# Kernel optimization log

Hardware: AMD Instinct MI355X
Metric: run time of the kernel (lower is better)

Reference implementation:

```python
import jax, jax.numpy as jnp
import numpy as np

B, N, I = 8, 1024, 64
E, H, D = 2, 2, 128   # edge types, heads per layer, hidden dim
O = 64                # num_outputs
IN1 = E * H * D       # layer-1 filter input dim (concat of layer-0 heads)


def setup_inputs() -> dict:
    key = jax.random.key(0)
    ks = jax.random.split(key, 20)
    s = lambda f: 1.0 / np.sqrt(f)
    inp = {
        "nodes": jax.random.normal(ks[0], (B, N, I), jnp.float32),
        "edges": jax.random.normal(ks[1], (B, N, N, E), jnp.float32) * 0.1,
        "Wemb": jax.random.normal(ks[2], (I, D), jnp.float32) * s(I),
        "bemb": jnp.zeros((D,), jnp.float32),
        # layer 0 params: filter W, att nets a1/a2 (weight + bias), state bias
        "W0":   jax.random.normal(ks[3], (E, H, D, D), jnp.float32) * s(D),
        "A1w0": jax.random.normal(ks[4], (E, H, D), jnp.float32) * s(D),
        "A1b0": jnp.zeros((E, H), jnp.float32),
        "A2w0": jax.random.normal(ks[5], (E, H, D), jnp.float32) * s(D),
        "A2b0": jnp.zeros((E, H), jnp.float32),
        "SB0":  jnp.zeros((E, H, D), jnp.float32),
        # layer 1 params (input dim = E*H*D from concat)
        "W1":   jax.random.normal(ks[6], (E, H, IN1, D), jnp.float32) * s(IN1),
        "A1w1": jax.random.normal(ks[7], (E, H, D), jnp.float32) * s(D),
        "A1b1": jnp.zeros((E, H), jnp.float32),
        "A2w1": jax.random.normal(ks[8], (E, H, D), jnp.float32) * s(D),
        "A2b1": jnp.zeros((E, H), jnp.float32),
        "SB1":  jnp.zeros((E, H, D), jnp.float32),
        "Wout": jax.random.normal(ks[9], (D, O), jnp.float32) * s(D),
        "bout": jnp.zeros((O,), jnp.float32),
    }
    return inp


def _gat_layer(state, edges_ebnn, W, a1w, a1b, a2w, a2b, sb):
    # state: (B,N,Fin); W: (E,H,Fin,D); edges_ebnn: (E,1,B,N,N)
    Wh = jnp.einsum('bni,ehid->ehbnd', state, W)                    # (E,H,B,N,D)
    s1 = jnp.einsum('ehbnd,ehd->ehbn', Wh, a1w) + a1b[:, :, None, None]
    s2 = jnp.einsum('ehbnd,ehd->ehbn', Wh, a2w) + a2b[:, :, None, None]
    att = s1[..., :, None] + s2[..., None, :]                       # a1_i + a2_j
    att = jax.nn.leaky_relu(att, 0.2) + edges_ebnn                  # edge-type bias
    att = jax.nn.softmax(att, axis=-2)                              # torch dim=1 (over i)
    msg = jnp.einsum('ehbij,ehbjd->ehbid', att, Wh)                 # bmm aggregation
    return msg + sb[:, :, None, None, :]                            # (E,H,B,N,D)


def reference(nodes, edges, Wemb, bemb,
              W0, A1w0, A1b0, A2w0, A2b0, SB0,
              W1, A1w1, A1b1, A2w1, A2b1, SB1,
              Wout, bout):
    edges_e = jnp.transpose(edges, (3, 0, 1, 2))[:, None]           # (E,1,B,N,N)
    state = jax.nn.relu(nodes @ Wemb + bemb)                        # SlimFC embedding
    # layer 0: concat heads/edgetypes along feature dim (torch order jj outer, ii inner)
    m0 = _gat_layer(state, edges_e, W0, A1w0, A1b0, A2w0, A2b0, SB0)
    state = jnp.transpose(m0, (2, 3, 0, 1, 4)).reshape(B, N, E * H * D)
    # layer 1 (last): elu then mean over all heads/edgetypes
    m1 = jax.nn.elu(_gat_layer(state, edges_e, W1, A1w1, A1b1, A2w1, A2b1, SB1))
    state = jnp.mean(m1, axis=(0, 1))                               # (B,N,D)
    return state @ Wout + bout                                      # (B,N,O)
```

## Files before the change

### kernel.cpp

```cpp
#include <hip/hip_runtime.h>
#include <math.h>

#define NB 8
#define NN 1024
#define NI 64
#define EHC 4
#define ND 128
#define NO 64
#define FIN1 512
#define BN 8192
#define LOG2E 1.4426950408889634f

typedef __attribute__((ext_vector_type(8))) short short8;
typedef __attribute__((ext_vector_type(4))) float f32x4;
typedef __attribute__((ext_vector_type(2))) unsigned uint32x2;

__device__ __forceinline__ unsigned short f2bf(float f) {
    union { float f; unsigned u; } v; v.f = f;
    unsigned r = v.u + 0x7FFF + ((v.u >> 16) & 1);
    return (unsigned short)(r >> 16);
}
__device__ __forceinline__ unsigned short f2h(float f) {
    union { _Float16 h; unsigned short u; } v;
    v.h = (_Float16)f;
    return v.u;
}
__device__ __forceinline__ float h2f(unsigned short u) {
    union { unsigned short u; _Float16 h; } v;
    v.u = u;
    return (float)v.h;
}

__global__ void prepTk(const float* __restrict__ W0, const float* __restrict__ W1,
                       const float* __restrict__ Wemb, const float* __restrict__ Wout,
                       unsigned short* __restrict__ W0T, unsigned short* __restrict__ W1T,
                       unsigned short* __restrict__ WembT, unsigned short* __restrict__ WoutT) {
    int idx = blockIdx.x * 256 + threadIdx.x;
    if (idx < EHC * ND * ND) {
        int eh = idx >> 14, d = (idx >> 7) & 127, k = idx & 127;
        W0T[idx] = f2bf(W0[((size_t)(eh * ND + k)) * ND + d]);
    }
    int idx1 = idx - EHC * ND * ND;
    if (idx1 >= 0 && idx1 < EHC * ND * FIN1) {
        int eh = idx1 >> 16;
        int r = idx1 & 65535;
        int d = r >> 9, k = r & 511;
        W1T[idx1] = f2bf(W1[((size_t)(eh * FIN1 + k)) * ND + d]);
    }
    int idx2 = idx - (EHC * ND * ND + EHC * ND * FIN1);
    if (idx2 >= 0 && idx2 < ND * NI) {
        int d = idx2 >> 6, k = idx2 & 63;
        WembT[idx2] = f2bf(Wemb[k * ND + d]);
    }
    int idx3 = idx - (EHC * ND * ND + EHC * ND * FIN1 + ND * NI);
    if (idx3 >= 0 && idx3 < ND * NO) {
        int o = idx3 >> 7, d = idx3 & 127;
        WoutT[idx3] = f2bf(Wout[d * NO + o]);
    }
}

__global__ __launch_bounds__(256, 4) void embwh0k(
    const float* __restrict__ nodes, const unsigned short* __restrict__ WembT,
    const float* __restrict__ bemb, const unsigned short* __restrict__ W0T,
    unsigned short* __restrict__ WhT, const float* __restrict__ a1w,
    const float* __restrict__ a1b, const float* __restrict__ a2w,
    const float* __restrict__ a2b, float* __restrict__ s1, float* __restrict__ s2) {
    int id = blockIdx.x;
    int g = id & 7, s_ = id >> 3;
    int eh = s_ & 3;
    int row0 = ((s_ >> 2) * 8 + g) * 32;
    int t = threadIdx.x;
    int w = t >> 6, lane = t & 63;
    int m = lane & 15, quad = lane >> 4;

    __shared__ unsigned short stateL[32 * 136];

    f32x4 accE[2][2];
#pragma unroll
    for (int mt = 0; mt < 2; ++mt)
#pragma unroll
        for (int nt = 0; nt < 2; ++nt) accE[mt][nt] = (f32x4){0.f, 0.f, 0.f, 0.f};
#pragma unroll
    for (int kt = 0; kt < 2; ++kt) {
        short8 aE[2], bE[2];
#pragma unroll
        for (int mt = 0; mt < 2; ++mt) {
            const float* np = nodes + (size_t)(row0 + mt * 16 + m) * NI + kt * 32 + quad * 8;
            f32x4 v0 = *(const f32x4*)np;
            f32x4 v1 = *(const f32x4*)(np + 4);
            union { unsigned short us[8]; short8 s8; } pk;
#pragma unroll
            for (int r = 0; r < 4; ++r) {
                pk.us[r] = f2bf(v0[r]);
                pk.us[r + 4] = f2bf(v1[r]);
            }
            aE[mt] = pk.s8;
        }
#pragma unroll
        for (int nt = 0; nt < 2; ++nt)
            bE[nt] = *(const short8*)(WembT + (w * 32 + nt * 16 + m) * NI + kt * 32 + quad * 8);
#pragma unroll
        for (int mt = 0; mt < 2; ++mt)
#pragma unroll
            for (int nt = 0; nt < 2; ++nt)
                accE[mt][nt] =
                    __builtin_amdgcn_mfma_f32_16x16x32_bf16(aE[mt], bE[nt], accE[mt][nt], 0, 0, 0);
    }
#pragma unroll
    for (int mt = 0; mt < 2; ++mt)
#pragma unroll
        for (int nt = 0; nt < 2; ++nt) {
            int d = w * 32 + nt * 16 + m;
            float bb = bemb[d];
#pragma unroll
            for (int r = 0; r < 4; ++r) {
                float v = fmaxf(accE[mt][nt][r] + bb, 0.f);
                stateL[(mt * 16 + quad * 4 + r) * 136 + d] = f2bf(v);
            }
        }
    __syncthreads();

    f32x4 acc[2][2];
#pragma unroll
    for (int mt = 0; mt < 2; ++mt)
#pragma unroll
        for (int nt = 0; nt < 2; ++nt) acc[mt][nt] = (f32x4){0.f, 0.f, 0.f, 0.f};
#pragma unroll
    for (int k0 = 0; k0 < ND; k0 += 32) {
        short8 a[2], b[2];
#pragma unroll
        for (int mt = 0; mt < 2; ++mt)
            a[mt] = *(const short8*)&stateL[(mt * 16 + m) * 136 + k0 + quad * 8];
#pragma unroll
        for (int nt = 0; nt < 2; ++nt)
            b[nt] = *(const short8*)(W0T + ((size_t)(eh * ND + w * 32 + nt * 16 + m)) * ND +
                                     k0 + quad * 8);
#pragma unroll
        for (int mt = 0; mt < 2; ++mt)
#pragma unroll
            for (int nt = 0; nt < 2; ++nt)
                acc[mt][nt] =
                    __builtin_amdgcn_mfma_f32_16x16x32_bf16(a[mt], b[nt], acc[mt][nt], 0, 0, 0);
    }

    int b_ = row0 >> 10, i0b = row0 & 1023;
    int ehb = eh * NB + b_;
#pragma unroll
    for (int mt = 0; mt < 2; ++mt)
#pragma unroll
        for (int nt = 0; nt < 2; ++nt) {
            int d = w * 32 + nt * 16 + m;
            int i = i0b + mt * 16 + quad * 4;
            union { unsigned short us[4]; unsigned long long u64; } pk;
#pragma unroll
            for (int r = 0; r < 4; ++r) pk.us[r] = f2bf(acc[mt][nt][r]);
            *(unsigned long long*)(WhT + (((size_t)ehb) * ND + d) * NN + i) = pk.u64;
        }
    float w1a = a1w[eh * ND + w * 32 + m], w1b = a1w[eh * ND + w * 32 + 16 + m];
    float w2a = a2w[eh * ND + w * 32 + m], w2b = a2w[eh * ND + w * 32 + 16 + m];
    float p1[2][4], p2[2][4];
#pragma unroll
    for (int mt = 0; mt < 2; ++mt)
#pragma unroll
        for (int r = 0; r < 4; ++r) {
            p1[mt][r] = acc[mt][0][r] * w1a + acc[mt][1][r] * w1b;
            p2[mt][r] = acc[mt][0][r] * w2a + acc[mt][1][r] * w2b;
        }
#pragma unroll
    for (int off = 8; off >= 1; off >>= 1)
#pragma unroll
        for (int mt = 0; mt < 2; ++mt)
#pragma unroll
            for (int r = 0; r < 4; ++r) {
                p1[mt][r] += __shfl_xor(p1[mt][r], off);
                p2[mt][r] += __shfl_xor(p2[mt][r], off);
            }
    __shared__ float sred[2][4][4][8];
    if (m == 0) {
#pragma unroll
        for (int mt = 0; mt < 2; ++mt)
#pragma unroll
            for (int r = 0; r < 4; ++r) {
                sred[0][w][quad][mt * 4 + r] = p1[mt][r];
                sred[1][w][quad][mt * 4 + r] = p2[mt][r];
            }
    }
    __syncthreads();
    if (t < 32) {
        int mt = t >> 4, quad2 = (t >> 2) & 3, r = t & 3;
        int c = mt * 4 + r;
        float v = sred[0][0][quad2][c] + sred[0][1][quad2][c] + sred[0][2][quad2][c] +
                  sred[0][3][quad2][c];
        s1[(size_t)ehb * NN + i0b + t] = (v + a1b[eh]) * LOG2E;
    } else if (t < 64) {
        int tl = t - 32;
        int mt = tl >> 4, quad2 = (tl >> 2) & 3, r = tl & 3;
        int c = mt * 4 + r;
        float v = sred[1][0][quad2][c] + sred[1][1][quad2][c] + sred[1][2][quad2][c] +
                  sred[1][3][quad2][c];
        s2[(size_t)ehb * NN + i0b + tl] = (v + a2b[eh]) * LOG2E;
    }
}

__global__ __launch_bounds__(256, 4) void whgemm1k(
    const unsigned short* __restrict__ state, const unsigned short* __restrict__ WT,
    unsigned short* __restrict__ WhT, const float* __restrict__ a1w,
    const float* __restrict__ a1b, const float* __restrict__ a2w,
    const float* __restrict__ a2b, float* __restrict__ s1, float* __restrict__ s2,
    float* __restrict__ outz) {
    int id = blockIdx.x;
    int g = id & 7, s_ = id >> 3;
    int eh = s_ & 3;
    int row0 = ((s_ >> 2) * 8 + g) * 32;
    int t = threadIdx.x;
    int w = t >> 6, lane = t & 63;
    int m = lane & 15, quad = lane >> 4;

    {
        f32x4 z = (f32x4){0.f, 0.f, 0.f, 0.f};
        for (int idx = t; idx < 128; idx += 256) ((f32x4*)outz)[(size_t)id * 128 + idx] = z;
    }

    f32x4 acc[2][2];
#pragma unroll
    for (int mt = 0; mt < 2; ++mt)
#pragma unroll
        for (int nt = 0; nt < 2; ++nt) acc[mt][nt] = (f32x4){0.f, 0.f, 0.f, 0.f};

    const unsigned short* Ab = state + (size_t)(row0 + m) * FIN1 + quad * 8;
    const unsigned short* Bb = WT + ((size_t)eh * ND + w * 32 + m) * FIN1 + quad * 8;
#pragma unroll 4
    for (int k0 = 0; k0 < FIN1; k0 += 32) {
        short8 a[2], b[2];
#pragma unroll
        for (int mt = 0; mt < 2; ++mt)
            a[mt] = *(const short8*)(Ab + (size_t)mt * 16 * FIN1 + k0);
#pragma unroll
        for (int nt = 0; nt < 2; ++nt)
            b[nt] = *(const short8*)(Bb + (size_t)nt * 16 * FIN1 + k0);
#pragma unroll
        for (int mt = 0; mt < 2; ++mt)
#pragma unroll
            for (int nt = 0; nt < 2; ++nt)
                acc[mt][nt] =
                    __builtin_amdgcn_mfma_f32_16x16x32_bf16(a[mt], b[nt], acc[mt][nt], 0, 0, 0);
    }
    int b_ = row0 >> 10, i0b = row0 & 1023;
    int ehb = eh * NB + b_;
#pragma unroll
    for (int mt = 0; mt < 2; ++mt)
#pragma unroll
        for (int nt = 0; nt < 2; ++nt) {
            int d = w * 32 + nt * 16 + m;
            int i = i0b + mt * 16 + quad * 4;
            union { unsigned short us[4]; unsigned long long u64; } pk;
#pragma unroll
            for (int r = 0; r < 4; ++r) pk.us[r] = f2bf(acc[mt][nt][r]);
            *(unsigned long long*)(WhT + (((size_t)ehb) * ND + d) * NN + i) = pk.u64;
        }
    float w1a = a1w[eh * ND + w * 32 + m], w1b = a1w[eh * ND + w * 32 + 16 + m];
    float w2a = a2w[eh * ND + w * 32 + m], w2b = a2w[eh * ND + w * 32 + 16 + m];
    float p1[2][4], p2[2][4];
#pragma unroll
    for (int mt = 0; mt < 2; ++mt)
#pragma unroll
        for (int r = 0; r < 4; ++r) {
            p1[mt][r] = acc[mt][0][r] * w1a + acc[mt][1][r] * w1b;
            p2[mt][r] = acc[mt][0][r] * w2a + acc[mt][1][r] * w2b;
        }
#pragma unroll
    for (int off = 8; off >= 1; off >>= 1)
#pragma unroll
        for (int mt = 0; mt < 2; ++mt)
#pragma unroll
            for (int r = 0; r < 4; ++r) {
                p1[mt][r] += __shfl_xor(p1[mt][r], off);
                p2[mt][r] += __shfl_xor(p2[mt][r], off);
            }
    __shared__ float sred[2][4][4][8];
    if (m == 0) {
#pragma unroll
        for (int mt = 0; mt < 2; ++mt)
#pragma unroll
            for (int r = 0; r < 4; ++r) {
                sred[0][w][quad][mt * 4 + r] = p1[mt][r];
                sred[1][w][quad][mt * 4 + r] = p2[mt][r];
            }
    }
    __syncthreads();
    if (t < 32) {
        int mt = t >> 4, quad2 = (t >> 2) & 3, r = t & 3;
        int c = mt * 4 + r;
        float v = sred[0][0][quad2][c] + sred[0][1][quad2][c] + sred[0][2][quad2][c] +
                  sred[0][3][quad2][c];
        s1[(size_t)ehb * NN + i0b + t] = (v + a1b[eh]) * LOG2E;
    } else if (t < 64) {
        int tl = t - 32;
        int mt = tl >> 4, quad2 = (tl >> 2) & 3, r = tl & 3;
        int c = mt * 4 + r;
        float v = sred[1][0][quad2][c] + sred[1][1][quad2][c] + sred[1][2][quad2][c] +
                  sred[1][3][quad2][c];
        s2[(size_t)ehb * NN + i0b + tl] = (v + a2b[eh]) * LOG2E;
    }
}

template <int CONV>
__global__ __launch_bounds__(256, 4) void colsumk(const float* __restrict__ edges,
                                                  unsigned* __restrict__ edgesH,
                                                  const float* __restrict__ s1,
                                                  const float* __restrict__ s2,
                                                  float* __restrict__ Spart) {
    int jt = blockIdx.x, b = blockIdx.y, ic = blockIdx.z;
    int t = threadIdx.x;
    int jp = t & 31, is = t >> 5;
    int j = jt * 64 + jp * 2;
    __shared__ float s1L[4][128];
    for (int idx = t; idx < 512; idx += 256) {
        int eh = idx >> 7;
        s1L[eh][idx & 127] = s1[((size_t)eh * NB + b) * NN + ic * 128 + (idx & 127)];
    }
    __syncthreads();
    float s2v[4][2], acc4[4][2];
#pragma unroll
    for (int eh = 0; eh < 4; ++eh) {
        s2v[eh][0] = s2[((size_t)eh * NB + b) * NN + j];
        s2v[eh][1] = s2[((size_t)eh * NB + b) * NN + j + 1];
        acc4[eh][0] = 0.f;
        acc4[eh][1] = 0.f;
    }
    int irow0 = ic * 128 + is * 16;
    const float4* ep = (const float4*)edges + (size_t)(b * NN + irow0) * (NN / 2) + jt * 32 + jp;
    unsigned* ehw = edgesH + (size_t)(b * NN + irow0) * NN + j;
#pragma unroll 4
    for (int ii = 0; ii < 16; ++ii) {
        float e00, e10, e01, e11;
        if (CONV) {
            float4 ev = ep[(size_t)ii * (NN / 2)];
            unsigned p0 = (unsigned)f2h(ev.x * LOG2E) | ((unsigned)f2h(ev.y * LOG2E) << 16);
            unsigned p1 = (unsigned)f2h(ev.z * LOG2E) | ((unsigned)f2h(ev.w * LOG2E) << 16);
            *(uint32x2*)(ehw + (size_t)ii * NN) = (uint32x2){p0, p1};
            e00 = h2f((unsigned short)(p0 & 0xffff));
            e10 = h2f((unsigned short)(p0 >> 16));
            e01 = h2f((unsigned short)(p1 & 0xffff));
            e11 = h2f((unsigned short)(p1 >> 16));
        } else {
            uint32x2 pk = *(const uint32x2*)(ehw + (size_t)ii * NN);
            e00 = h2f((unsigned short)(pk.x & 0xffff));
            e10 = h2f((unsigned short)(pk.x >> 16));
            e01 = h2f((unsigned short)(pk.y & 0xffff));
            e11 = h2f((unsigned short)(pk.y >> 16));
        }
#pragma unroll
        for (int eh = 0; eh < 4; ++eh) {
            float sv = s1L[eh][is * 16 + ii];
            float x0 = sv + s2v[eh][0];
            x0 = fmaxf(x0, 0.2f * x0);
            acc4[eh][0] += __builtin_exp2f(x0 + (eh < 2 ? e00 : e10));
            float x1 = sv + s2v[eh][1];
            x1 = fmaxf(x1, 0.2f * x1);
            acc4[eh][1] += __builtin_exp2f(x1 + (eh < 2 ? e01 : e11));
        }
    }
    __shared__ float red[8][4][64];
#pragma unroll
    for (int eh = 0; eh < 4; ++eh) {
        red[is][eh][jp * 2] = acc4[eh][0];
        red[is][eh][jp * 2 + 1] = acc4[eh][1];
    }
    __syncthreads();
    if (t < 256) {
        int eho = t >> 6, jlo = t & 63;
        float Sv = 0.f;
#pragma unroll
        for (int isx = 0; isx < 8; ++isx) Sv += red[isx][eho][jlo];
        Spart[(((size_t)ic * EHC + eho) * NB + b) * NN + jt * 64 + jlo] = Sv;
    }
}

__global__ __launch_bounds__(512, 8) void msgk(const unsigned* __restrict__ edgesH,
                                               const unsigned short* __restrict__ WhT,
                                               const float* __restrict__ s1,
                                               const float* __restrict__ s2,
                                               const float* __restrict__ Spart,
                                               const float* __restrict__ sb,
                                               unsigned short* __restrict__ out0,
                                               const unsigned short* __restrict__ WoutT,
                                               const float* __restrict__ bout,
                                               float* __restrict__ out, int mode) {
    int id = blockIdx.x;
    int b = id & 7;
    int s_ = id >> 3;
    int eh = s_ & 3;
    int itile = s_ >> 2;
    int e = eh >> 1;
    int i0 = itile * 32;
    int t = threadIdx.x;
    int w = t >> 6, lane = t & 63;
    int n = lane & 15, quad = lane >> 4;
    int jl = t & 63, ib = w;

    __shared__ float2 stL[NN];
    __shared__ unsigned short pA[2][32 * 72];

    int base = (eh * NB + b) * NN;
    const size_t pstr = (size_t)EHC * NB * NN;
    for (int jj = t; jj < NN; jj += 512) {
        float S = 0.f;
#pragma unroll
        for (int ic = 0; ic < 8; ++ic) S += Spart[(size_t)ic * pstr + base + jj];
        stL[jj] = make_float2(s2[base + jj], __builtin_log2f(S));
    }
    float s1r[4];
    {
        f32x4 v0 = *(const f32x4*)(s1 + base + i0 + ib * 4);
#pragma unroll
        for (int r = 0; r < 4; ++r) s1r[r] = v0[r];
    }

    f32x4 acc[2];
#pragma unroll
    for (int nt = 0; nt < 2; ++nt) acc[nt] = (f32x4){0.f, 0.f, 0.f, 0.f};

    const unsigned short* Ab =
        WhT + ((size_t)base * ND + (size_t)(w * 16 + n) * NN) + quad * 8;
    const unsigned* ep = edgesH + (size_t)(b * NN + i0 + ib * 4) * NN + jl;
    __syncthreads();

    unsigned evA[4], evB[4];
    short8 aA[2], aB[2];

    auto loadE = [&](unsigned* ev, int j0) {
#pragma unroll
        for (int q = 0; q < 4; ++q) ev[q] = ep[(size_t)q * NN + j0];
    };
    auto loadA = [&](short8* av, int j0) {
#pragma unroll
        for (int kt = 0; kt < 2; ++kt)
            av[kt] = *(const short8*)(Ab + kt * 32 + j0);
    };
    auto pstep = [&](const unsigned* ev, const short8* av, int j0, int buf) {
        float2 stj = stL[j0 + jl];
#pragma unroll
        for (int q = 0; q < 4; ++q) {
            float edge = h2f((unsigned short)(e ? (ev[q] >> 16) : (ev[q] & 0xffff)));
            float x = s1r[q] + stj.x;
            x = fmaxf(x, 0.2f * x);
            pA[buf][(ib * 4 + q) * 72 + jl] = f2bf(__builtin_exp2f(x + edge - stj.y));
        }
        __syncthreads();
#pragma unroll
        for (int kt = 0; kt < 2; ++kt) {
            short8 bv[2];
#pragma unroll
            for (int nt = 0; nt < 2; ++nt)
                bv[nt] = *(const short8*)&pA[buf][(nt * 16 + n) * 72 + kt * 32 + quad * 8];
#pragma unroll
            for (int nt = 0; nt < 2; ++nt)
                acc[nt] =
                    __builtin_amdgcn_mfma_f32_16x16x32_bf16(av[kt], bv[nt], acc[nt], 0, 0, 0);
        }
    };

    loadE(evA, 0);
    loadA(aA, 0);
    for (int sp2 = 0; sp2 < 8; ++sp2) {
        int j0 = sp2 * 128;
        loadE(evB, j0 + 64);
        loadA(aB, j0 + 64);
        pstep(evA, aA, j0, 0);
        if (sp2 < 7) {
            loadE(evA, j0 + 128);
            loadA(aA, j0 + 128);
        }
        pstep(evB, aB, j0 + 64, 1);
    }

    int d0 = w * 16 + quad * 4;
    f32x4 sbv = *(const f32x4*)&sb[eh * ND + d0];
    if (mode == 0) {
#pragma unroll
        for (int nt = 0; nt < 2; ++nt) {
            int i = i0 + nt * 16 + n;
            union { unsigned short us[4]; unsigned long long u64; } pk;
#pragma unroll
            for (int r = 0; r < 4; ++r) pk.us[r] = f2bf(acc[nt][r] + sbv[r]);
            *(unsigned long long*)(out0 + (size_t)(b * NN + i) * FIN1 + eh * ND + d0) = pk.u64;
        }
    } else {
        __syncthreads();
        unsigned short* eluL = (unsigned short*)pA;
#pragma unroll
        for (int nt = 0; nt < 2; ++nt) {
            int il = nt * 16 + n;
#pragma unroll
            for (int r = 0; r < 4; ++r) {
                float v = acc[nt][r] + sbv[r];
                v = v > 0.f ? v : expm1f(v);
                eluL[il * 136 + d0 + r] = f2bf(v);
            }
        }
        __syncthreads();
        int it = w & 1, ot = w >> 1;
        f32x4 hacc = (f32x4){0.f, 0.f, 0.f, 0.f};
#pragma unroll
        for (int k0 = 0; k0 < ND; k0 += 32) {
            short8 av = *(const short8*)&eluL[(it * 16 + n) * 136 + k0 + quad * 8];
            short8 bv = *(const short8*)(WoutT + (ot * 16 + n) * ND + k0 + quad * 8);
            hacc = __builtin_amdgcn_mfma_f32_16x16x32_bf16(av, bv, hacc, 0, 0, 0);
        }
        int o = ot * 16 + n;
        float bo = bout[o];
        float* op = out + (size_t)(b * NN + i0 + it * 16 + quad * 4) * NO + o;
#pragma unroll
        for (int r = 0; r < 4; ++r)
            atomicAdd(op + (size_t)r * NO, 0.25f * hacc[r] + 0.25f * bo);
    }
}

extern "C" void kernel_launch(void* const* d_in, const int* in_sizes, int n_in,
                              void* d_out, int out_size, void* d_ws, size_t ws_size,
                              hipStream_t stream) {
    const float* nodes = (const float*)d_in[0];
    const float* edges = (const float*)d_in[1];
    const float* Wemb = (const float*)d_in[2];
    const float* bemb = (const float*)d_in[3];
    const float* W0 = (const float*)d_in[4];
    const float* A1w0 = (const float*)d_in[5];
    const float* A1b0 = (const float*)d_in[6];
    const float* A2w0 = (const float*)d_in[7];
    const float* A2b0 = (const float*)d_in[8];
    const float* SB0 = (const float*)d_in[9];
    const float* W1 = (const float*)d_in[10];
    const float* A1w1 = (const float*)d_in[11];
    const float* A1b1 = (const float*)d_in[12];
    const float* A2w1 = (const float*)d_in[13];
    const float* A2b1 = (const float*)d_in[14];
    const float* SB1 = (const float*)d_in[15];
    const float* Wout = (const float*)d_in[16];
    const float* bout = (const float*)d_in[17];
    float* out = (float*)d_out;

    char* p = (char*)d_ws;
    auto alloc = [&](size_t bytes) {
        char* r = p;
        p += (bytes + 255) & ~(size_t)255;
        return r;
    };
    unsigned short* W0T = (unsigned short*)alloc((size_t)EHC * ND * ND * 2);
    unsigned short* W1T = (unsigned short*)alloc((size_t)EHC * ND * FIN1 * 2);
    unsigned short* WembT = (unsigned short*)alloc((size_t)ND * NI * 2);
    unsigned short* WoutT = (unsigned short*)alloc((size_t)ND * NO * 2);
    unsigned short* WhT = (unsigned short*)alloc((size_t)EHC * BN * ND * 2);
    unsigned short* state1 = (unsigned short*)alloc((size_t)BN * FIN1 * 2);
    float* s1b = (float*)alloc((size_t)EHC * BN * 4);
    float* s2b = (float*)alloc((size_t)EHC * BN * 4);
    float* Spart = (float*)alloc((size_t)8 * EHC * BN * 4);
    unsigned* edgesH = (unsigned*)alloc((size_t)NB * NN * NN * 4);

    prepTk<<<1344, 256, 0, stream>>>(W0, W1, Wemb, Wout, W0T, W1T, WembT, WoutT);
    embwh0k<<<1024, 256, 0, stream>>>(nodes, WembT, bemb, W0T, WhT, A1w0, A1b0, A2w0, A2b0,
                                      s1b, s2b);
    colsumk<1><<<dim3(NN / 64, NB, 8), 256, 0, stream>>>(edges, edgesH, s1b, s2b, Spart);
    msgk<<<1024, 512, 0, stream>>>(edgesH, WhT, s1b, s2b, Spart, SB0, state1, WoutT, bout,
                                   out, 0);
    whgemm1k<<<1024, 256, 0, stream>>>(state1, W1T, WhT, A1w1, A1b1, A2w1, A2b1, s1b, s2b,
                                       out);
    colsumk<0><<<dim3(NN / 64, NB, 8), 256, 0, stream>>>(edges, edgesH, s1b, s2b, Spart);
    msgk<<<1024, 512, 0, stream>>>(edgesH, WhT, s1b, s2b, Spart, SB1, state1, WoutT, bout,
                                   out, 1);
}
```

Before: 281.4 us.

## Split edge planes per type and compute attention probabilities in registers for MFMA

The half-precision edge cache is split into one plane per edge type instead of interleaving both types in each 32-bit word. The message kernel now reads only the plane it needs and builds bf16 attention probabilities directly in MFMA operand registers, so the shared-memory staging buffer and the per-step barriers go away. It also changes the block shape: 256 threads, each wave owns 32 rows by 64 features, and the grid is halved. The aim is to cut edge-read bandwidth and LDS traffic, at the cost of more registers per thread and lower occupancy.

```diff
diff --git a/kernel.cpp b/kernel.cpp
--- a/kernel.cpp
+++ b/kernel.cpp
@@ -13,7 +13,6 @@
 
 typedef __attribute__((ext_vector_type(8))) short short8;
 typedef __attribute__((ext_vector_type(4))) float f32x4;
-typedef __attribute__((ext_vector_type(2))) unsigned uint32x2;
 
 __device__ __forceinline__ unsigned short f2bf(float f) {
     union { float f; unsigned u; } v; v.f = f;
@@ -306,10 +305,11 @@
 
 template <int CONV>
 __global__ __launch_bounds__(256, 4) void colsumk(const float* __restrict__ edges,
-                                                  unsigned* __restrict__ edgesH,
+                                                  unsigned short* __restrict__ edgesP,
                                                   const float* __restrict__ s1,
                                                   const float* __restrict__ s2,
                                                   float* __restrict__ Spart) {
+    const size_t PO = (size_t)NB * NN * NN;
     int jt = blockIdx.x, b = blockIdx.y, ic = blockIdx.z;
     int t = threadIdx.x;
     int jp = t & 31, is = t >> 5;
@@ -330,35 +330,31 @@
     }
     int irow0 = ic * 128 + is * 16;
     const float4* ep = (const float4*)edges + (size_t)(b * NN + irow0) * (NN / 2) + jt * 32 + jp;
-    unsigned* ehw = edgesH + (size_t)(b * NN + irow0) * NN + j;
+    unsigned short* pb = edgesP + (size_t)(b * NN + irow0) * NN + j;
 #pragma unroll 4
     for (int ii = 0; ii < 16; ++ii) {
-        float e00, e10, e01, e11;
+        unsigned q0, q1;
         if (CONV) {
             float4 ev = ep[(size_t)ii * (NN / 2)];
-            unsigned p0 = (unsigned)f2h(ev.x * LOG2E) | ((unsigned)f2h(ev.y * LOG2E) << 16);
-            unsigned p1 = (unsigned)f2h(ev.z * LOG2E) | ((unsigned)f2h(ev.w * LOG2E) << 16);
-            *(uint32x2*)(ehw + (size_t)ii * NN) = (uint32x2){p0, p1};
-            e00 = h2f((unsigned short)(p0 & 0xffff));
-            e10 = h2f((unsigned short)(p0 >> 16));
-            e01 = h2f((unsigned short)(p1 & 0xffff));
-            e11 = h2f((unsigned short)(p1 >> 16));
+            q0 = (unsigned)f2h(ev.x * LOG2E) | ((unsigned)f2h(ev.z * LOG2E) << 16);
+            q1 = (unsigned)f2h(ev.y * LOG2E) | ((unsigned)f2h(ev.w * LOG2E) << 16);
+            *(unsigned*)(pb + (size_t)ii * NN) = q0;
+            *(unsigned*)(pb + PO + (size_t)ii * NN) = q1;
         } else {
-            uint32x2 pk = *(const uint32x2*)(ehw + (size_t)ii * NN);
-            e00 = h2f((unsigned short)(pk.x & 0xffff));
-            e10 = h2f((unsigned short)(pk.x >> 16));
-            e01 = h2f((unsigned short)(pk.y & 0xffff));
-            e11 = h2f((unsigned short)(pk.y >> 16));
-        }
+            q0 = *(const unsigned*)(pb + (size_t)ii * NN);
+            q1 = *(const unsigned*)(pb + PO + (size_t)ii * NN);
+        }
+        float p0lo = h2f((unsigned short)(q0 & 0xffff)), p0hi = h2f((unsigned short)(q0 >> 16));
+        float p1lo = h2f((unsigned short)(q1 & 0xffff)), p1hi = h2f((unsigned short)(q1 >> 16));
 #pragma unroll
         for (int eh = 0; eh < 4; ++eh) {
             float sv = s1L[eh][is * 16 + ii];
             float x0 = sv + s2v[eh][0];
             x0 = fmaxf(x0, 0.2f * x0);
-            acc4[eh][0] += __builtin_exp2f(x0 + (eh < 2 ? e00 : e10));
+            acc4[eh][0] += __builtin_exp2f(x0 + (eh < 2 ? p0lo : p1lo));
             float x1 = sv + s2v[eh][1];
             x1 = fmaxf(x1, 0.2f * x1);
-            acc4[eh][1] += __builtin_exp2f(x1 + (eh < 2 ? e01 : e11));
+            acc4[eh][1] += __builtin_exp2f(x1 + (eh < 2 ? p0hi : p1hi));
         }
     }
     __shared__ float red[8][4][64];
@@ -377,7 +373,7 @@
     }
 }
 
-__global__ __launch_bounds__(512, 8) void msgk(const unsigned* __restrict__ edgesH,
+__global__ __launch_bounds__(256, 2) void msgk(const unsigned short* __restrict__ edgesP,
                                                const unsigned short* __restrict__ WhT,
                                                const float* __restrict__ s1,
                                                const float* __restrict__ s2,
@@ -393,127 +389,116 @@
     int eh = s_ & 3;
     int itile = s_ >> 2;
     int e = eh >> 1;
-    int i0 = itile * 32;
     int t = threadIdx.x;
     int w = t >> 6, lane = t & 63;
     int n = lane & 15, quad = lane >> 4;
-    int jl = t & 63, ib = w;
+    int dh = w & 1, isub = w >> 1;
+    int i0w = itile * 64 + isub * 32;
 
     __shared__ float2 stL[NN];
-    __shared__ unsigned short pA[2][32 * 72];
+    __shared__ unsigned short eluL[2][32][136];
 
     int base = (eh * NB + b) * NN;
     const size_t pstr = (size_t)EHC * NB * NN;
-    for (int jj = t; jj < NN; jj += 512) {
+    for (int jj = t; jj < NN; jj += 256) {
         float S = 0.f;
 #pragma unroll
         for (int ic = 0; ic < 8; ++ic) S += Spart[(size_t)ic * pstr + base + jj];
-        stL[jj] = make_float2(s2[base + jj], __builtin_log2f(S));
-    }
-    float s1r[4];
-    {
-        f32x4 v0 = *(const f32x4*)(s1 + base + i0 + ib * 4);
-#pragma unroll
-        for (int r = 0; r < 4; ++r) s1r[r] = v0[r];
-    }
-
-    f32x4 acc[2];
-#pragma unroll
-    for (int nt = 0; nt < 2; ++nt) acc[nt] = (f32x4){0.f, 0.f, 0.f, 0.f};
-
-    const unsigned short* Ab =
-        WhT + ((size_t)base * ND + (size_t)(w * 16 + n) * NN) + quad * 8;
-    const unsigned* ep = edgesH + (size_t)(b * NN + i0 + ib * 4) * NN + jl;
+        stL[jj] = make_float2(s2[base + jj], -__builtin_log2f(S));
+    }
+    float s1r0 = s1[base + i0w + n];
+    float s1r1 = s1[base + i0w + 16 + n];
     __syncthreads();
 
-    unsigned evA[4], evB[4];
-    short8 aA[2], aB[2];
-
-    auto loadE = [&](unsigned* ev, int j0) {
-#pragma unroll
-        for (int q = 0; q < 4; ++q) ev[q] = ep[(size_t)q * NN + j0];
-    };
-    auto loadA = [&](short8* av, int j0) {
-#pragma unroll
-        for (int kt = 0; kt < 2; ++kt)
-            av[kt] = *(const short8*)(Ab + kt * 32 + j0);
-    };
-    auto pstep = [&](const unsigned* ev, const short8* av, int j0, int buf) {
-        float2 stj = stL[j0 + jl];
-#pragma unroll
-        for (int q = 0; q < 4; ++q) {
-            float edge = h2f((unsigned short)(e ? (ev[q] >> 16) : (ev[q] & 0xffff)));
-            float x = s1r[q] + stj.x;
-            x = fmaxf(x, 0.2f * x);
-            pA[buf][(ib * 4 + q) * 72 + jl] = f2bf(__builtin_exp2f(x + edge - stj.y));
-        }
+    f32x4 acc[2][4];
+#pragma unroll
+    for (int bf = 0; bf < 2; ++bf)
+#pragma unroll
+        for (int dt = 0; dt < 4; ++dt) acc[bf][dt] = (f32x4){0.f, 0.f, 0.f, 0.f};
+
+    const unsigned short* Ap =
+        WhT + ((size_t)base * ND + (size_t)(dh * 64 + n) * NN) + quad * 8;
+    const unsigned short* Ep =
+        edgesP + ((size_t)(e * NB + b) * NN + i0w + n) * NN + quad * 8;
+
+    for (int kc = 0; kc < 32; ++kc) {
+        int j0 = kc * 32;
+        short8 a[4];
+#pragma unroll
+        for (int dt = 0; dt < 4; ++dt)
+            a[dt] = *(const short8*)(Ap + (size_t)(dt * 16) * NN + j0);
+        short8 ev0 = *(const short8*)(Ep + j0);
+        short8 ev1 = *(const short8*)(Ep + (size_t)16 * NN + j0);
+        float2 stj[8];
+#pragma unroll
+        for (int r = 0; r < 8; ++r) stj[r] = stL[j0 + quad * 8 + r];
+        union { unsigned short us[8]; short8 s8; } pk0, pk1;
+#pragma unroll
+        for (int r = 0; r < 8; ++r) {
+            float x0 = s1r0 + stj[r].x;
+            x0 = fmaxf(x0, 0.2f * x0);
+            x0 += h2f((unsigned short)ev0[r]) + stj[r].y;
+            pk0.us[r] = f2bf(__builtin_exp2f(x0));
+            float x1 = s1r1 + stj[r].x;
+            x1 = fmaxf(x1, 0.2f * x1);
+            x1 += h2f((unsigned short)ev1[r]) + stj[r].y;
+            pk1.us[r] = f2bf(__builtin_exp2f(x1));
+        }
+#pragma unroll
+        for (int dt = 0; dt < 4; ++dt) {
+            acc[0][dt] = __builtin_amdgcn_mfma_f32_16x16x32_bf16(a[dt], pk0.s8, acc[0][dt], 0, 0, 0);
+            acc[1][dt] = __builtin_amdgcn_mfma_f32_16x16x32_bf16(a[dt], pk1.s8, acc[1][dt], 0, 0, 0);
+        }
+    }
+
+    if (mode == 0) {
+#pragma unroll
+        for (int bf = 0; bf < 2; ++bf)
+#pragma unroll
+            for (int dt = 0; dt < 4; ++dt) {
+                int d0g = dh * 64 + dt * 16 + quad * 4;
+                int i = i0w + bf * 16 + n;
+                f32x4 sbv = *(const f32x4*)&sb[eh * ND + d0g];
+                union { unsigned short us[4]; unsigned long long u64; } pk;
+#pragma unroll
+                for (int r = 0; r < 4; ++r) pk.us[r] = f2bf(acc[bf][dt][r] + sbv[r]);
+                *(unsigned long long*)(out0 + (size_t)(b * NN + i) * FIN1 + eh * ND + d0g) =
+                    pk.u64;
+            }
+    } else {
+#pragma unroll
+        for (int bf = 0; bf < 2; ++bf)
+#pragma unroll
+            for (int dt = 0; dt < 4; ++dt) {
+                int dloc = dh * 64 + dt * 16 + quad * 4;
+                f32x4 sbv = *(const f32x4*)&sb[eh * ND + dloc];
+                union { unsigned short us[4]; unsigned long long u64; } pk;
+#pragma unroll
+                for (int r = 0; r < 4; ++r) {
+                    float v = acc[bf][dt][r] + sbv[r];
+                    pk.us[r] = f2bf(v > 0.f ? v : expm1f(v));
+                }
+                *(unsigned long long*)&eluL[isub][bf * 16 + n][dloc] = pk.u64;
+            }
         __syncthreads();
 #pragma unroll
-        for (int kt = 0; kt < 2; ++kt) {
-            short8 bv[2];
-#pragma unroll
-            for (int nt = 0; nt < 2; ++nt)
-                bv[nt] = *(const short8*)&pA[buf][(nt * 16 + n) * 72 + kt * 32 + quad * 8];
-#pragma unroll
-            for (int nt = 0; nt < 2; ++nt)
-                acc[nt] =
-                    __builtin_amdgcn_mfma_f32_16x16x32_bf16(av[kt], bv[nt], acc[nt], 0, 0, 0);
-        }
-    };
-
-    loadE(evA, 0);
-    loadA(aA, 0);
-    for (int sp2 = 0; sp2 < 8; ++sp2) {
-        int j0 = sp2 * 128;
-        loadE(evB, j0 + 64);
-        loadA(aB, j0 + 64);
-        pstep(evA, aA, j0, 0);
-        if (sp2 < 7) {
-            loadE(evA, j0 + 128);
-            loadA(aA, j0 + 128);
-        }
-        pstep(evB, aB, j0 + 64, 1);
-    }
-
-    int d0 = w * 16 + quad * 4;
-    f32x4 sbv = *(const f32x4*)&sb[eh * ND + d0];
-    if (mode == 0) {
-#pragma unroll
-        for (int nt = 0; nt < 2; ++nt) {
-            int i = i0 + nt * 16 + n;
-            union { unsigned short us[4]; unsigned long long u64; } pk;
-#pragma unroll
-            for (int r = 0; r < 4; ++r) pk.us[r] = f2bf(acc[nt][r] + sbv[r]);
-            *(unsigned long long*)(out0 + (size_t)(b * NN + i) * FIN1 + eh * ND + d0) = pk.u64;
-        }
-    } else {
-        __syncthreads();
-        unsigned short* eluL = (unsigned short*)pA;
-#pragma unroll
-        for (int nt = 0; nt < 2; ++nt) {
-            int il = nt * 16 + n;
-#pragma unroll
-            for (int r = 0; r < 4; ++r) {
-                float v = acc[nt][r] + sbv[r];
-                v = v > 0.f ? v : expm1f(v);
-                eluL[il * 136 + d0 + r] = f2bf(v);
-            }
-        }
-        __syncthreads();
-        int it = w & 1, ot = w >> 1;
-        f32x4 hacc = (f32x4){0.f, 0.f, 0.f, 0.f};
-#pragma unroll
-        for (int k0 = 0; k0 < ND; k0 += 32) {
-            short8 av = *(const short8*)&eluL[(it * 16 + n) * 136 + k0 + quad * 8];
-            short8 bv = *(const short8*)(WoutT + (ot * 16 + n) * ND + k0 + quad * 8);
-            hacc = __builtin_amdgcn_mfma_f32_16x16x32_bf16(av, bv, hacc, 0, 0, 0);
-        }
-        int o = ot * 16 + n;
-        float bo = bout[o];
-        float* op = out + (size_t)(b * NN + i0 + it * 16 + quad * 4) * NO + o;
-#pragma unroll
-        for (int r = 0; r < 4; ++r)
-            atomicAdd(op + (size_t)r * NO, 0.25f * hacc[r] + 0.25f * bo);
+        for (int it = 0; it < 2; ++it)
+#pragma unroll
+            for (int ot = 0; ot < 2; ++ot) {
+                int o = (dh * 2 + ot) * 16 + n;
+                f32x4 hacc = (f32x4){0.f, 0.f, 0.f, 0.f};
+#pragma unroll
+                for (int k0 = 0; k0 < 4; ++k0) {
+                    short8 av = *(const short8*)&eluL[isub][it * 16 + n][k0 * 32 + quad * 8];
+                    short8 bv = *(const short8*)(WoutT + (size_t)o * ND + k0 * 32 + quad * 8);
+                    hacc = __builtin_amdgcn_mfma_f32_16x16x32_bf16(av, bv, hacc, 0, 0, 0);
+                }
+                float bo = bout[o];
+                float* op = out + (size_t)(b * NN + i0w + it * 16 + quad * 4) * NO + o;
+#pragma unroll
+                for (int r = 0; r < 4; ++r)
+                    atomicAdd(op + (size_t)r * NO, 0.25f * hacc[r] + 0.25f * bo);
+            }
     }
 }
 
@@ -555,17 +540,17 @@
     float* s1b = (float*)alloc((size_t)EHC * BN * 4);
     float* s2b = (float*)alloc((size_t)EHC * BN * 4);
     float* Spart = (float*)alloc((size_t)8 * EHC * BN * 4);
-    unsigned* edgesH = (unsigned*)alloc((size_t)NB * NN * NN * 4);
+    unsigned short* edgesP = (unsigned short*)alloc((size_t)2 * NB * NN * NN * 2);
 
     prepTk<<<1344, 256, 0, stream>>>(W0, W1, Wemb, Wout, W0T, W1T, WembT, WoutT);
     embwh0k<<<1024, 256, 0, stream>>>(nodes, WembT, bemb, W0T, WhT, A1w0, A1b0, A2w0, A2b0,
                                       s1b, s2b);
-    colsumk<1><<<dim3(NN / 64, NB, 8), 256, 0, stream>>>(edges, edgesH, s1b, s2b, Spart);
-    msgk<<<1024, 512, 0, stream>>>(edgesH, WhT, s1b, s2b, Spart, SB0, state1, WoutT, bout,
-                                   out, 0);
+    colsumk<1><<<dim3(NN / 64, NB, 8), 256, 0, stream>>>(edges, edgesP, s1b, s2b, Spart);
+    msgk<<<512, 256, 0, stream>>>(edgesP, WhT, s1b, s2b, Spart, SB0, state1, WoutT, bout,
+                                  out, 0);
     whgemm1k<<<1024, 256, 0, stream>>>(state1, W1T, WhT, A1w1, A1b1, A2w1, A2b1, s1b, s2b,
                                        out);
-    colsumk<0><<<dim3(NN / 64, NB, 8), 256, 0, stream>>>(edges, edgesH, s1b, s2b, Spart);
-    msgk<<<1024, 512, 0, stream>>>(edgesH, WhT, s1b, s2b, Spart, SB1, state1, WoutT, bout,
-                                   out, 1);
-}
+    colsumk<0><<<dim3(NN / 64, NB, 8), 256, 0, stream>>>(edges, edgesP, s1b, s2b, Spart);
+    msgk<<<512, 256, 0, stream>>>(edgesP, WhT, s1b, s2b, Spart, SB1, state1, WoutT, bout,
+                                  out, 1);
+}
```

After: 302.1 us. +7.3%, slower.
